# Performance work log

Hardware: AMD Instinct MI355X
Metric: run time of the kernel (lower is better)

Reference implementation:

```python
import jax, jax.numpy as jnp
import numpy as np

B, S, D = 2, 2048, 1024
H, DH, DL = 16, 64, 512
E, DFF, K = 8, 2048, 2
EPS = 1e-5


def setup_inputs() -> dict:
    key = jax.random.key(0)
    ks = jax.random.split(key, 10)
    std = 0.02
    inp = {
        'x': jax.random.normal(ks[0], (B, S, D), jnp.float32),
        'mask': jnp.tril(jnp.ones((S, S), dtype=bool))[None, None],  # causal (1,1,S,S)
        'ln1_scale': jnp.ones((D,), jnp.float32),
        'ln1_bias': jnp.zeros((D,), jnp.float32),
        'Wq': jax.random.normal(ks[1], (D, H * DH), jnp.float32) * std,
        'Wdkv': jax.random.normal(ks[2], (D, DL), jnp.float32) * std,
        'Wukv': jax.random.normal(ks[3], (DL, H * DH), jnp.float32) * std,
        'Wo': jax.random.normal(ks[4], (H * DH, D), jnp.float32) * std,
        'ln2_scale': jnp.ones((D,), jnp.float32),
        'ln2_bias': jnp.zeros((D,), jnp.float32),
        'Wgate': jax.random.normal(ks[5], (D, E), jnp.float32) * std,
        'bgate': jnp.zeros((E,), jnp.float32),
        'We1': jax.random.normal(ks[6], (E, D, DFF), jnp.float32) * std,
        'be1': jnp.zeros((E, DFF), jnp.float32),
        'We2': jax.random.normal(ks[7], (E, DFF, D), jnp.float32) * std,
        'be2': jnp.zeros((E, D), jnp.float32),
    }
    return inp


def _layernorm(x, g, b):
    m = jnp.mean(x, axis=-1, keepdims=True)
    v = jnp.mean(jnp.square(x - m), axis=-1, keepdims=True)
    return (x - m) * jax.lax.rsqrt(v + EPS) * g + b


def reference(x, mask, ln1_scale, ln1_bias, Wq, Wdkv, Wukv, Wo,
              ln2_scale, ln2_bias, Wgate, bgate, We1, be1, We2, be2):
    b, s, d = x.shape
    # --- MLA attention ---
    h = _layernorm(x, ln1_scale, ln1_bias)
    q = (h @ Wq).reshape(b, s, H, DH)
    kv = ((h @ Wdkv) @ Wukv).reshape(b, s, H, DH)  # k == v == kv
    scores = jnp.einsum('bqhd,bkhd->bhqk', q, kv) / (DH ** 0.5)
    scores = jnp.where(mask, scores, -jnp.inf)
    probs = jax.nn.softmax(scores, axis=-1)
    attn = jnp.einsum('bhqk,bkhd->bqhd', probs, kv).reshape(b, s, H * DH)
    x = x + attn @ Wo
    # --- MoE ---
    h2 = _layernorm(x, ln2_scale, ln2_bias)
    xf = h2.reshape(-1, d)                     # (T, D)
    T = xf.shape[0]
    logits = xf @ Wgate + bgate                # (T, E)
    w, sel = jax.lax.top_k(logits, K)          # (T, K)
    w = jax.nn.softmax(w, axis=-1)
    # scatter top-k weights into dense (T, E) combine weights
    wfull = jnp.zeros((T, E), xf.dtype).at[jnp.arange(T)[:, None], sel].add(w)
    hid = jax.nn.gelu(jnp.einsum('td,edf->etf', xf, We1) + be1[:, None, :],
                      approximate=False)
    oute = jnp.einsum('etf,efd->etd', hid, We2) + be2[:, None, :]
    moe = jnp.einsum('te,etd->td', wfull, oute)
    return x + moe.reshape(b, s, d)
```

## Files before the change

kernel.cpp:

```cpp
#include <hip/hip_runtime.h>

#define EPS_LN 1e-5f

typedef __attribute__((ext_vector_type(4))) float f32x4;
typedef __attribute__((ext_vector_type(8))) __bf16 bf16x8;
typedef __attribute__((ext_vector_type(2))) unsigned int u32x2;
typedef unsigned int u32;
typedef unsigned short u16;

__device__ __forceinline__ u16 f2b(float f) {
  unsigned int u = __builtin_bit_cast(unsigned int, f);
  unsigned int r = (u + 0x7FFFu + ((u >> 16) & 1u)) >> 16;
  return (u16)r;
}
__device__ __forceinline__ float b2f(u16 s) {
  unsigned int u = ((unsigned int)s) << 16;
  return __builtin_bit_cast(float, u);
}
__device__ __forceinline__ void splitf(float v, u16& h, u16& l) {
  h = f2b(v); l = f2b(v - b2f(h));
}
__device__ __forceinline__ float gelu_exact(float v) {
  return 0.5f * v * (1.0f + erff(v * 0.70710678118654752440f));
}
__device__ __forceinline__ void gload16(const void* g, void* l) {
  __builtin_amdgcn_global_load_lds((const __attribute__((address_space(1))) u32*)g,
                                   (__attribute__((address_space(3))) u32*)l, 16, 0, 0);
}
__device__ __forceinline__ void pv_mfma(f32x4& o, u32x2 a, u32x2 b) {
  asm("s_nop 1\n\tv_mfma_f32_16x16x16_bf16 %0, %1, %2, %0" : "+v"(o) : "v"(a), "v"(b));
}
__device__ __forceinline__ int fsw(int row, int sc) {
  return row * 64 + ((((sc >> 3) ^ (row & 7))) << 3) + (sc & 7);
}

__global__ __launch_bounds__(256) void k_transpose_bf16(
    const float* __restrict__ src, u16* __restrict__ dst, int K, int N)
{
  __shared__ u16 t[64][65];
  long base = (long)blockIdx.z * (long)K * (long)N;
  const float* s = src + base;
  u16* d = dst + base;
  int n0 = blockIdx.x * 64, k0 = blockIdx.y * 64;
  int c = threadIdx.x & 63, r = threadIdx.x >> 6;
#pragma unroll
  for (int i = 0; i < 16; i++) {
    int k = r * 16 + i;
    t[c][k] = f2b(s[(long)(k0 + k) * N + n0 + c]);
  }
  __syncthreads();
#pragma unroll
  for (int i = 0; i < 16; i++) {
    int n = r * 16 + i;
    d[(long)(n0 + n) * K + k0 + c] = t[n][c];
  }
}

__global__ __launch_bounds__(256) void k_split_transpose(
    const float* __restrict__ src, u16* __restrict__ dh,
    u16* __restrict__ dl, int K, int N)
{
  __shared__ float t[64][65];
  int n0 = blockIdx.x * 64, k0 = blockIdx.y * 64;
  int c = threadIdx.x & 63, r4 = threadIdx.x >> 6;
#pragma unroll
  for (int i = 0; i < 16; i++) {
    int k = r4 * 16 + i;
    t[c][k] = src[(long)(k0 + k) * N + n0 + c];
  }
  __syncthreads();
#pragma unroll
  for (int i = 0; i < 16; i++) {
    int n = r4 * 16 + i;
    float v = t[n][c];
    u16 h = f2b(v);
    dh[(long)(n0 + n) * K + k0 + c] = h;
    dl[(long)(n0 + n) * K + k0 + c] = f2b(v - b2f(h));
  }
}

__global__ __launch_bounds__(256) void k_transpose_kv(
    const u16* __restrict__ inh, const u16* __restrict__ inl,
    u16* __restrict__ outh, u16* __restrict__ outl)
{
  __shared__ u16 th[64][65];
  __shared__ u16 tl[64][65];
  int bh = blockIdx.y, s0 = blockIdx.x * 64;
  int b = bh >> 4, h = bh & 15;
  int c = threadIdx.x & 63, r = threadIdx.x >> 6;
  long ibase = ((long)b * 2048 + s0) * 1024 + h * 64;
  long obase = (long)bh * 64 * 2048 + s0;
#pragma unroll
  for (int i = 0; i < 16; i++) {
    int k = r * 16 + i;
    th[c][k] = inh[ibase + (long)k * 1024 + c];
    tl[c][k] = inl[ibase + (long)k * 1024 + c];
  }
  __syncthreads();
#pragma unroll
  for (int i = 0; i < 16; i++) {
    int n = r * 16 + i;
    outh[obase + (long)n * 2048 + c] = th[n][c];
    outl[obase + (long)n * 2048 + c] = tl[n][c];
  }
}

template<int MODE>
__global__ __launch_bounds__(256) void k_layernorm(
    const float* __restrict__ x, const float* __restrict__ g,
    const float* __restrict__ b, u16* __restrict__ o1, u16* __restrict__ o2)
{
  int row = blockIdx.x, tid = threadIdx.x;
  const float* xr = x + (long)row * 1024;
  float4 v = *(const float4*)&xr[tid * 4];
  float s = v.x + v.y + v.z + v.w;
  float sq = v.x * v.x + v.y * v.y + v.z * v.z + v.w * v.w;
#pragma unroll
  for (int o = 32; o; o >>= 1) { s += __shfl_down(s, o); sq += __shfl_down(sq, o); }
  __shared__ float red[8];
  int wave = tid >> 6, lane = tid & 63;
  if (lane == 0) { red[wave] = s; red[4 + wave] = sq; }
  __syncthreads();
  s  = red[0] + red[1] + red[2] + red[3];
  sq = red[4] + red[5] + red[6] + red[7];
  float mean = s * (1.0f / 1024.0f);
  float var  = sq * (1.0f / 1024.0f) - mean * mean;
  float rs = rsqrtf(var + EPS_LN);
  float4 gg = *(const float4*)&g[tid * 4];
  float4 bb = *(const float4*)&b[tid * 4];
  float ov[4];
  ov[0] = (v.x - mean) * rs * gg.x + bb.x;
  ov[1] = (v.y - mean) * rs * gg.y + bb.y;
  ov[2] = (v.z - mean) * rs * gg.z + bb.z;
  ov[3] = (v.w - mean) * rs * gg.w + bb.w;
  if (MODE == 1) {
    ushort4 o4; o4.x = f2b(ov[0]); o4.y = f2b(ov[1]); o4.z = f2b(ov[2]); o4.w = f2b(ov[3]);
    *(ushort4*)&o1[(long)row * 1024 + tid * 4] = o4;
  } else {
    ushort4 hh, ll;
    splitf(ov[0], hh.x, ll.x); splitf(ov[1], hh.y, ll.y);
    splitf(ov[2], hh.z, ll.z); splitf(ov[3], hh.w, ll.w);
    *(ushort4*)&o1[(long)row * 1024 + tid * 4] = hh;
    *(ushort4*)&o2[(long)row * 1024 + tid * 4] = ll;
  }
}

__global__ __launch_bounds__(256) void k_gemm_bf3(
    const u16* __restrict__ Ah, const u16* __restrict__ Al,
    const u16* __restrict__ Bh, const u16* __restrict__ Bl,
    float* __restrict__ P, int M, int N, int K)
{
  int split = blockIdx.x & 1;
  int bid = blockIdx.x >> 1;
  int nwg = gridDim.x >> 1, cpx = nwg >> 3;
  int wg = (bid & 7) * cpx + (bid >> 3);
  int mm = M >> 7;
  int mb = wg % mm, nb = wg / mm;
  long m0 = (long)mb * 128, n0 = (long)nb * 128;
  int K2 = K >> 1;
  int kbase = split * K2;
  __shared__ __align__(16) u16 sA[2][128 * 64];
  __shared__ __align__(16) u16 sB[2][128 * 64];
  int tid = threadIdx.x, lane = tid & 63, w = tid >> 6;
  int wr = w >> 1, wc = w & 1, l15 = lane & 15, l4 = lane >> 4;
  int lr8 = lane >> 3;
  int cl = (lane & 7) ^ lr8;
  int scol = (cl & 3) * 8;
  const u16* bA = (cl < 4) ? Ah : Al;
  const u16* bB = (cl < 4) ? Bh : Bl;
  long a_off[4], b_off[4];
#pragma unroll
  for (int r = 0; r < 4; r++) {
    int row = w * 32 + r * 8 + lr8;
    a_off[r] = (m0 + row) * (long)K + kbase + scol;
    b_off[r] = (n0 + row) * (long)K + kbase + scol;
  }
  int nt = K2 >> 5;

  f32x4 acc[4][4];
  f32x4 zz = {0.0f, 0.0f, 0.0f, 0.0f};
#pragma unroll
  for (int i = 0; i < 4; i++)
#pragma unroll
    for (int j = 0; j < 4; j++) acc[i][j] = zz;

#define STAGE_BF3(buf, s_) do { long o = (long)(s_) * 32; \
    _Pragma("unroll") \
    for (int r = 0; r < 4; r++) { \
      gload16(&bA[a_off[r] + o], &sA[buf][(w * 32 + r * 8) * 64]); \
      gload16(&bB[b_off[r] + o], &sB[buf][(w * 32 + r * 8) * 64]); \
    } } while (0)

  STAGE_BF3(0, 0);
  __syncthreads();
  int cur = 0;
  for (int s = 0; s < nt; s++) {
    if (s + 1 < nt) STAGE_BF3(cur ^ 1, s + 1);
    bf16x8 ah[4], al[4], bh[4], bl[4];
#pragma unroll
    for (int mi = 0; mi < 4; mi++) {
      int row = wr * 64 + mi * 16 + l15;
      int k7 = l15 & 7;
      ah[mi] = *(const bf16x8*)&sA[cur][row * 64 + ((l4 ^ k7) * 8)];
      al[mi] = *(const bf16x8*)&sA[cur][row * 64 + (((4 + l4) ^ k7) * 8)];
    }
#pragma unroll
    for (int ni = 0; ni < 4; ni++) {
      int row = wc * 64 + ni * 16 + l15;
      int k7 = l15 & 7;
      bh[ni] = *(const bf16x8*)&sB[cur][row * 64 + ((l4 ^ k7) * 8)];
      bl[ni] = *(const bf16x8*)&sB[cur][row * 64 + (((4 + l4) ^ k7) * 8)];
    }
#pragma unroll
    for (int mi = 0; mi < 4; mi++)
#pragma unroll
      for (int ni = 0; ni < 4; ni++) {
        acc[mi][ni] = __builtin_amdgcn_mfma_f32_16x16x32_bf16(ah[mi], bh[ni], acc[mi][ni], 0, 0, 0);
        acc[mi][ni] = __builtin_amdgcn_mfma_f32_16x16x32_bf16(ah[mi], bl[ni], acc[mi][ni], 0, 0, 0);
        acc[mi][ni] = __builtin_amdgcn_mfma_f32_16x16x32_bf16(al[mi], bh[ni], acc[mi][ni], 0, 0, 0);
      }
    __syncthreads();
    cur ^= 1;
  }
#undef STAGE_BF3
  long base = (long)split * M * N;
#pragma unroll
  for (int mi = 0; mi < 4; mi++) {
#pragma unroll
    for (int j = 0; j < 4; j++) {
      long row = m0 + wr * 64 + mi * 16 + l4 * 4 + j;
#pragma unroll
      for (int ni = 0; ni < 4; ni++) {
        long col = n0 + wc * 64 + ni * 16 + l15;
        P[base + row * N + col] = acc[mi][ni][j];
      }
    }
  }
}

__global__ __launch_bounds__(256) void k_red_split(
    const float* __restrict__ P, u16* __restrict__ Ch, u16* __restrict__ Cl, long MN)
{
  long i = ((long)blockIdx.x * 256 + threadIdx.x) * 4;
  float4 a = *(const float4*)&P[i];
  float4 b = *(const float4*)&P[MN + i];
  ushort4 h, l;
  splitf(a.x + b.x, h.x, l.x); splitf(a.y + b.y, h.y, l.y);
  splitf(a.z + b.z, h.z, l.z); splitf(a.w + b.w, h.w, l.w);
  *(ushort4*)&Ch[i] = h;
  *(ushort4*)&Cl[i] = l;
}

__global__ __launch_bounds__(256) void k_red_resid(
    const float* __restrict__ P, const float* __restrict__ x,
    float* __restrict__ out, long MN)
{
  long i = ((long)blockIdx.x * 256 + threadIdx.x) * 4;
  float4 a = *(const float4*)&P[i];
  float4 b = *(const float4*)&P[MN + i];
  float4 xv = *(const float4*)&x[i];
  float4 r = {a.x + b.x + xv.x, a.y + b.y + xv.y, a.z + b.z + xv.z, a.w + b.w + xv.w};
  *(float4*)&out[i] = r;
}

__global__ __launch_bounds__(256) void k_flash_v3(
    const u16* __restrict__ Qh, const u16* __restrict__ Ql,
    const u16* __restrict__ Kh, const u16* __restrict__ Kl,
    const u16* __restrict__ Th, const u16* __restrict__ Tl,
    u16* __restrict__ Oh, u16* __restrict__ Ol)
{
  int qb = (int)gridDim.y - 1 - (int)blockIdx.y;
  int bh = blockIdx.x;
  int q0 = qb * 64;
  int tid = threadIdx.x, lane = tid & 63, w = tid >> 6;
  int l15 = lane & 15, l4 = lane >> 4;
  __shared__ __align__(16) u16 Qsh[4096], Qsl[4096];
  __shared__ __align__(16) u16 Ksh[2][4096], Ksl[2][4096];
  __shared__ __align__(16) u16 Tsh[2][4096], Tsl[2][4096];
  long rowb = (long)(bh >> 4) * 2048;
  int  colo = (bh & 15) * 64;
  long tbase = (long)bh * 64 * 2048;
  int r8 = lane >> 3;
  int c8s = ((lane & 7) ^ r8) * 8;

#pragma unroll
  for (int k = 0; k < 2; k++) {
    int rr = w * 16 + k * 8;
    long src = (rowb + q0 + rr + r8) * 1024 + colo + c8s;
    gload16(&Qh[src], &Qsh[rr * 64]);
    gload16(&Ql[src], &Qsl[rr * 64]);
  }
#pragma unroll
  for (int k = 0; k < 2; k++) {
    int rr = w * 16 + k * 8;
    long srcK = (rowb + rr + r8) * 1024 + colo + c8s;
    long srcT = tbase + (long)(rr + r8) * 2048 + c8s;
    gload16(&Kh[srcK], &Ksh[0][rr * 64]);
    gload16(&Kl[srcK], &Ksl[0][rr * 64]);
    gload16(&Th[srcT], &Tsh[0][rr * 64]);
    gload16(&Tl[srcT], &Tsl[0][rr * 64]);
  }
  __syncthreads();

  float m = -1e30f, lsum = 0.0f;
  f32x4 o[4];
  f32x4 zz = {0.0f, 0.0f, 0.0f, 0.0f};
#pragma unroll
  for (int nb = 0; nb < 4; nb++) o[nb] = zz;
  int cur = 0;

  for (int kt = 0; kt <= qb; kt++) {
    int k0 = kt * 64;
    if (kt < qb) {
      int kn = k0 + 64, nxt = cur ^ 1;
#pragma unroll
      for (int k = 0; k < 2; k++) {
        int rr = w * 16 + k * 8;
        long srcK = (rowb + kn + rr + r8) * 1024 + colo + c8s;
        long srcT = tbase + (long)(rr + r8) * 2048 + kn + c8s;
        gload16(&Kh[srcK], &Ksh[nxt][rr * 64]);
        gload16(&Kl[srcK], &Ksl[nxt][rr * 64]);
        gload16(&Th[srcT], &Tsh[nxt][rr * 64]);
        gload16(&Tl[srcT], &Tsl[nxt][rr * 64]);
      }
    }
    f32x4 sT[4];
#pragma unroll
    for (int mi = 0; mi < 4; mi++) sT[mi] = zz;
#pragma unroll
    for (int ds = 0; ds < 2; ds++) {
      int qoff = fsw(w * 16 + l15, ds * 32 + l4 * 8);
      bf16x8 qh = *(const bf16x8*)&Qsh[qoff];
      bf16x8 ql = *(const bf16x8*)&Qsl[qoff];
#pragma unroll
      for (int mi = 0; mi < 4; mi++) {
        int koff = fsw(mi * 16 + l15, ds * 32 + l4 * 8);
        bf16x8 kh = *(const bf16x8*)&Ksh[cur][koff];
        bf16x8 kl = *(const bf16x8*)&Ksl[cur][koff];
        sT[mi] = __builtin_amdgcn_mfma_f32_16x16x32_bf16(kh, qh, sT[mi], 0, 0, 0);
        sT[mi] = __builtin_amdgcn_mfma_f32_16x16x32_bf16(kh, ql, sT[mi], 0, 0, 0);
        sT[mi] = __builtin_amdgcn_mfma_f32_16x16x32_bf16(kl, qh, sT[mi], 0, 0, 0);
      }
    }
    bool diag = (kt == qb);
    int qg = q0 + w * 16 + l15;
    float p[4][4];
    float tm = -1e30f;
#pragma unroll
    for (int mi = 0; mi < 4; mi++)
#pragma unroll
      for (int r = 0; r < 4; r++) {
        float v = sT[mi][r] * 0.125f;
        if (diag && (k0 + mi * 16 + l4 * 4 + r > qg)) v = -1e30f;
        p[mi][r] = v; tm = fmaxf(tm, v);
      }
    tm = fmaxf(tm, __shfl_xor(tm, 16));
    tm = fmaxf(tm, __shfl_xor(tm, 32));
    float mn = fmaxf(m, tm);
    float corr = __expf(m - mn);
    m = mn;
    float rs = 0.0f;
#pragma unroll
    for (int mi = 0; mi < 4; mi++)
#pragma unroll
      for (int r = 0; r < 4; r++) {
        float pv = __expf(p[mi][r] - mn);
        p[mi][r] = pv; rs += pv;
      }
    rs += __shfl_xor(rs, 16);
    rs += __shfl_xor(rs, 32);
    lsum = lsum * corr + rs;
    float corrO[4];
#pragma unroll
    for (int r = 0; r < 4; r++) corrO[r] = __shfl(corr, l4 * 4 + r);
#pragma unroll
    for (int nb = 0; nb < 4; nb++)
#pragma unroll
      for (int r = 0; r < 4; r++) o[nb][r] *= corrO[r];
    u32x2 pah[4], pal[4];
#pragma unroll
    for (int mi = 0; mi < 4; mi++) {
      u16 h[4], l[4];
#pragma unroll
      for (int r = 0; r < 4; r++) splitf(p[mi][r], h[r], l[r]);
      pah[mi][0] = (u32)h[0] | ((u32)h[1] << 16);
      pah[mi][1] = (u32)h[2] | ((u32)h[3] << 16);
      pal[mi][0] = (u32)l[0] | ((u32)l[1] << 16);
      pal[mi][1] = (u32)l[2] | ((u32)l[3] << 16);
    }
#pragma unroll
    for (int nb = 0; nb < 4; nb++) {
#pragma unroll
      for (int mi = 0; mi < 4; mi++) {
        int toff = fsw(nb * 16 + l15, mi * 16 + l4 * 4);
        u32x2 vh = *(const u32x2*)&Tsh[cur][toff];
        u32x2 vl = *(const u32x2*)&Tsl[cur][toff];
        pv_mfma(o[nb], pah[mi], vh);
        pv_mfma(o[nb], pah[mi], vl);
        pv_mfma(o[nb], pal[mi], vh);
      }
    }
    __syncthreads();
    cur ^= 1;
  }
  __builtin_amdgcn_sched_barrier(0);
  asm volatile("s_nop 7\n\ts_nop 7" ::: "memory");
  __builtin_amdgcn_sched_barrier(0);
  float inv[4];
#pragma unroll
  for (int r = 0; r < 4; r++) inv[r] = 1.0f / __shfl(lsum, l4 * 4 + r);
#pragma unroll
  for (int nb = 0; nb < 4; nb++)
#pragma unroll
    for (int r = 0; r < 4; r++) {
      long idx = (rowb + q0 + w * 16 + l4 * 4 + r) * 1024 + colo + nb * 16 + l15;
      u16 hh_, ll_; splitf(o[nb][r] * inv[r], hh_, ll_);
      Oh[idx] = hh_; Ol[idx] = ll_;
    }
}

__global__ __launch_bounds__(256) void k_gate(
    const float* __restrict__ x1, const float* __restrict__ g2, const float* __restrict__ b2,
    const float* __restrict__ Wg, const float* __restrict__ bg,
    int* __restrict__ sel, float* __restrict__ wts)
{
  int t = blockIdx.x * 4 + (threadIdx.x >> 6);
  int lane = threadIdx.x & 63;
  const float* xr = x1 + (long)t * 1024;
  float v[16], s = 0.0f, sq = 0.0f;
#pragma unroll
  for (int i = 0; i < 16; i++) { v[i] = xr[lane + 64 * i]; s += v[i]; sq += v[i] * v[i]; }
#pragma unroll
  for (int o = 32; o; o >>= 1) { s += __shfl_xor(s, o); sq += __shfl_xor(sq, o); }
  float mean = s * (1.0f / 1024.0f);
  float var = sq * (1.0f / 1024.0f) - mean * mean;
  float rs = rsqrtf(var + EPS_LN);
  float acc[8];
#pragma unroll
  for (int e = 0; e < 8; e++) acc[e] = 0.0f;
#pragma unroll
  for (int i = 0; i < 16; i++) {
    int d = lane + 64 * i;
    float hh = (v[i] - mean) * rs * g2[d] + b2[d];
    float4 w0 = *(const float4*)&Wg[d * 8];
    float4 w1 = *(const float4*)&Wg[d * 8 + 4];
    acc[0] += hh * w0.x; acc[1] += hh * w0.y; acc[2] += hh * w0.z; acc[3] += hh * w0.w;
    acc[4] += hh * w1.x; acc[5] += hh * w1.y; acc[6] += hh * w1.z; acc[7] += hh * w1.w;
  }
#pragma unroll
  for (int o = 32; o; o >>= 1)
#pragma unroll
    for (int e = 0; e < 8; e++) acc[e] += __shfl_xor(acc[e], o);
  if (lane == 0) {
    float le[8];
#pragma unroll
    for (int e = 0; e < 8; e++) le[e] = acc[e] + bg[e];
    int i0 = 0;
    for (int e = 1; e < 8; e++) if (le[e] > le[i0]) i0 = e;
    int i1 = (i0 == 0) ? 1 : 0;
    for (int e = 0; e < 8; e++) if (e != i0 && le[e] > le[i1]) i1 = e;
    float w0 = 1.0f / (1.0f + __expf(le[i1] - le[i0]));
    sel[2 * t] = i0; sel[2 * t + 1] = i1;
    wts[2 * t] = w0; wts[2 * t + 1] = 1.0f - w0;
  }
}

__global__ __launch_bounds__(256) void k_count(const int* __restrict__ sel, int* __restrict__ cnt)
{
  int e = blockIdx.x, tid = threadIdx.x;
  int c = 0;
  for (int t = tid; t < 4096; t += 256)
    c += (sel[2 * t] == e) + (sel[2 * t + 1] == e);
#pragma unroll
  for (int o = 32; o; o >>= 1) c += __shfl_down(c, o);
  __shared__ int red[4];
  int wave = tid >> 6, lane = tid & 63;
  if (lane == 0) red[wave] = c;
  __syncthreads();
  if (tid == 0) cnt[e] = red[0] + red[1] + red[2] + red[3];
}

__global__ void k_offsets(const int* __restrict__ cnt, int* __restrict__ offs)
{
  if (threadIdx.x == 0) {
    int a = 0; offs[0] = 0;
    for (int e = 0; e < 8; e++) { a += cnt[e]; offs[e + 1] = a; }
  }
}

__global__ __launch_bounds__(256) void k_scatter(
    const int* __restrict__ sel, const int* __restrict__ offs,
    int* __restrict__ tlist, int* __restrict__ slot_of)
{
  int e = blockIdx.x, tid = threadIdx.x;
  int lane = tid & 63, wave = tid >> 6;
  __shared__ int wsum[4];
  int base = offs[e];
  for (int t0 = 0; t0 < 4096; t0 += 256) {
    int t = t0 + tid;
    int s0 = sel[2 * t], s1 = sel[2 * t + 1];
    bool p = (s0 == e) || (s1 == e);
    int k = (s0 == e) ? 0 : 1;
    unsigned long long mb = __ballot(p);
    int rank = __popcll(mb & ((1ull << lane) - 1ull));
    if (lane == 0) wsum[wave] = __popcll(mb);
    __syncthreads();
    int wbase = 0;
    for (int w = 0; w < wave; w++) wbase += wsum[w];
    if (p) { int idx = base + wbase + rank; tlist[idx] = t; slot_of[2 * t + k] = idx; }
    base += wsum[0] + wsum[1] + wsum[2] + wsum[3];
    __syncthreads();
  }
}

template<int EPI>
__global__ __launch_bounds__(256) void k_gemm_moe(
    const u16* __restrict__ A, const u16* __restrict__ Bt,
    void* __restrict__ Cout, const float* __restrict__ bias,
    const int* __restrict__ tlist, const int* __restrict__ offs,
    int N, int K, long strideB, int strideBias)
{
  int e = blockIdx.x & 7, slot = blockIdx.x >> 3;
  int r0 = offs[e], r1 = offs[e + 1];
  int rows = r1 - r0;
  if (rows <= 0) return;
  int nn = N >> 7;
  int ntiles = ((rows + 127) >> 7) * nn;
  const u16* B = Bt + (long)e * strideB;
  const float* bvec = bias + (long)e * strideBias;
  __shared__ __align__(16) u16 lA[2][128 * 64];
  __shared__ __align__(16) u16 lB[2][128 * 64];
  int tid = threadIdx.x, lane = tid & 63, w = tid >> 6;
  int wr = w >> 1, wc = w & 1;
  int l15 = lane & 15, l4 = lane >> 4;
  int lr8 = lane >> 3;
  int csrc = ((lane & 7) ^ lr8) * 8;
  int nt = K >> 6;

  for (int t = slot; t < ntiles; t += 256) {
    int rbk = t / nn, nb = t - rbk * nn;
    int m0 = r0 + rbk * 128;
    long n0 = (long)nb * 128;
    u32 asrc[4], bsrc[4];
#pragma unroll
    for (int r = 0; r < 4; r++) {
      int row = w * 32 + r * 8 + lr8;
      int g = m0 + row; if (g > r1 - 1) g = r1 - 1;
      int ar = (EPI == 2) ? tlist[g] : g;
      asrc[r] = (u32)ar * (u32)K + csrc;
      bsrc[r] = (u32)(n0 + row) * (u32)K + csrc;
    }
    f32x4 acc[4][4];
    f32x4 zz = {0.0f, 0.0f, 0.0f, 0.0f};
#pragma unroll
    for (int i = 0; i < 4; i++)
#pragma unroll
      for (int j = 0; j < 4; j++) acc[i][j] = zz;

#define STAGE_MOE(buf, k0_) do { u32 o_ = (k0_); \
    _Pragma("unroll") \
    for (int r = 0; r < 4; r++) { \
      gload16(&A[asrc[r] + o_], &lA[buf][(w * 32 + r * 8) * 64]); \
      gload16(&B[bsrc[r] + o_], &lB[buf][(w * 32 + r * 8) * 64]); \
    } } while (0)

    STAGE_MOE(0, 0);
    __syncthreads();
    int cur = 0;
    for (int s = 0; s < nt; s++) {
      if (s + 1 < nt) STAGE_MOE(cur ^ 1, (u32)(s + 1) * 64);
#pragma unroll
      for (int ks = 0; ks < 2; ks++) {
        bf16x8 af[4], bq[4];
#pragma unroll
        for (int mi = 0; mi < 4; mi++) {
          int row = wr * 64 + mi * 16 + l15;
          af[mi] = *(const bf16x8*)&lA[cur][row * 64 + (((ks * 4 + l4) ^ (l15 & 7)) * 8)];
        }
#pragma unroll
        for (int ni = 0; ni < 4; ni++) {
          int row = wc * 64 + ni * 16 + l15;
          bq[ni] = *(const bf16x8*)&lB[cur][row * 64 + (((ks * 4 + l4) ^ (l15 & 7)) * 8)];
        }
#pragma unroll
        for (int mi = 0; mi < 4; mi++)
#pragma unroll
          for (int ni = 0; ni < 4; ni++)
            acc[mi][ni] = __builtin_amdgcn_mfma_f32_16x16x32_bf16(af[mi], bq[ni], acc[mi][ni], 0, 0, 0);
      }
      __syncthreads();
      cur ^= 1;
    }
#undef STAGE_MOE
#pragma unroll
    for (int mi = 0; mi < 4; mi++) {
#pragma unroll
      for (int j = 0; j < 4; j++) {
        int row = m0 + wr * 64 + mi * 16 + l4 * 4 + j;
        if (row < r1) {
#pragma unroll
          for (int ni = 0; ni < 4; ni++) {
            long col = n0 + wc * 64 + ni * 16 + l15;
            float vv = acc[mi][ni][j] + bvec[col];
            if (EPI == 2) {
              ((u16*)Cout)[(long)row * N + col] = f2b(gelu_exact(vv));
            } else {
              ((float*)Cout)[(long)row * N + col] = vv;
            }
          }
        }
      }
    }
  }
}

__global__ __launch_bounds__(256) void k_combine(
    const float* __restrict__ x1, const float* __restrict__ oute,
    const int* __restrict__ slot_of, const float* __restrict__ wts,
    float* __restrict__ out)
{
  int t = blockIdx.x;
  int c = threadIdx.x * 4;
  int s0 = slot_of[2 * t], s1 = slot_of[2 * t + 1];
  float w0 = wts[2 * t], w1 = wts[2 * t + 1];
  float4 a  = *(const float4*)&x1[(long)t * 1024 + c];
  float4 e0 = *(const float4*)&oute[(long)s0 * 1024 + c];
  float4 e1 = *(const float4*)&oute[(long)s1 * 1024 + c];
  float4 r;
  r.x = a.x + w0 * e0.x + w1 * e1.x;
  r.y = a.y + w0 * e0.y + w1 * e1.y;
  r.z = a.z + w0 * e0.z + w1 * e1.z;
  r.w = a.w + w0 * e0.w + w1 * e1.w;
  *(float4*)&out[(long)t * 1024 + c] = r;
}

extern "C" void kernel_launch(void* const* d_in, const int* in_sizes, int n_in,
                              void* d_out, int out_size, void* d_ws, size_t ws_size,
                              hipStream_t stream)
{
  const float* x    = (const float*)d_in[0];
  const float* ln1s = (const float*)d_in[2];
  const float* ln1b = (const float*)d_in[3];
  const float* Wq   = (const float*)d_in[4];
  const float* Wdkv = (const float*)d_in[5];
  const float* Wukv = (const float*)d_in[6];
  const float* Wo   = (const float*)d_in[7];
  const float* ln2s = (const float*)d_in[8];
  const float* ln2b = (const float*)d_in[9];
  const float* Wg   = (const float*)d_in[10];
  const float* bg   = (const float*)d_in[11];
  const float* We1  = (const float*)d_in[12];
  const float* be1  = (const float*)d_in[13];
  const float* We2  = (const float*)d_in[14];
  const float* be2  = (const float*)d_in[15];
  float* out = (float*)d_out;

  char* wp = (char*)d_ws;
  auto take = [&](size_t nbytes) -> void* {
    char* r = wp; wp += (nbytes + 255) & ~(size_t)255; return (void*)r;
  };
  u16* We1t = (u16*)take(8L * 2048 * 1024 * 2);
  u16* We2t = (u16*)take(8L * 1024 * 2048 * 2);
  u16* hh   = (u16*)take(4096L * 1024 * 2);
  u16* hl   = (u16*)take(4096L * 1024 * 2);
  u16* qh   = (u16*)take(4096L * 1024 * 2);
  u16* ql   = (u16*)take(4096L * 1024 * 2);
  u16* kvh  = (u16*)take(4096L * 1024 * 2);
  u16* kvl  = (u16*)take(4096L * 1024 * 2);
  u16* kvTh = (u16*)take(4096L * 1024 * 2);
  u16* kvTl = (u16*)take(4096L * 1024 * 2);
  u16* cbh  = (u16*)take(4096L * 512 * 2);
  u16* cbl  = (u16*)take(4096L * 512 * 2);
  float* x1 = (float*)take(4096L * 1024 * 4);
  u16* hid  = (u16*)take(8192L * 2048 * 2);
  int*   sel   = (int*)take(8192 * 4);
  float* wts   = (float*)take(8192 * 4);
  int*   cnt   = (int*)take(64);
  int*   offs  = (int*)take(64);
  int*   tlist = (int*)take(8192 * 4);
  int*   slot  = (int*)take(8192 * 4);
  u16* attn_h = hh;
  u16* attn_l = hl;
  u16* h2bf   = cbh;
  float* oute = (float*)qh;
  float* Pk   = (float*)We2t;
  u16* Wqh   = hid;
  u16* Wql   = Wqh   + 1024L * 1024;
  u16* Wdkvh = Wql   + 1024L * 1024;
  u16* Wdkvl = Wdkvh + 512L * 1024;
  u16* Wukvh = Wdkvl + 512L * 1024;
  u16* Wukvl = Wukvh + 1024L * 512;
  u16* Woh   = Wukvl + 1024L * 512;
  u16* Wol   = Woh   + 1024L * 1024;
  if ((size_t)(wp - (char*)d_ws) > ws_size) return;

  dim3 b256(256);
  k_split_transpose<<<dim3(16, 16), b256, 0, stream>>>(Wq,   Wqh,   Wql,   1024, 1024);
  k_split_transpose<<<dim3(8, 16),  b256, 0, stream>>>(Wdkv, Wdkvh, Wdkvl, 1024, 512);
  k_split_transpose<<<dim3(16, 8),  b256, 0, stream>>>(Wukv, Wukvh, Wukvl, 512, 1024);
  k_split_transpose<<<dim3(16, 16), b256, 0, stream>>>(Wo,   Woh,   Wol,   1024, 1024);
  k_layernorm<2><<<dim3(4096), b256, 0, stream>>>(x, ln1s, ln1b, hh, hl);
  k_gemm_bf3<<<dim3(512), b256, 0, stream>>>(hh, hl, Wqh, Wql, Pk, 4096, 1024, 1024);
  k_red_split<<<dim3(4096), b256, 0, stream>>>(Pk, qh, ql, 4096L * 1024);
  k_gemm_bf3<<<dim3(256), b256, 0, stream>>>(hh, hl, Wdkvh, Wdkvl, Pk, 4096, 512, 1024);
  k_red_split<<<dim3(2048), b256, 0, stream>>>(Pk, cbh, cbl, 4096L * 512);
  k_gemm_bf3<<<dim3(512), b256, 0, stream>>>(cbh, cbl, Wukvh, Wukvl, Pk, 4096, 1024, 512);
  k_red_split<<<dim3(4096), b256, 0, stream>>>(Pk, kvh, kvl, 4096L * 1024);
  k_transpose_kv<<<dim3(32, 32), b256, 0, stream>>>(kvh, kvl, kvTh, kvTl);
  k_flash_v3<<<dim3(32, 32), b256, 0, stream>>>(qh, ql, kvh, kvl, kvTh, kvTl, attn_h, attn_l);
  k_gemm_bf3<<<dim3(512), b256, 0, stream>>>(attn_h, attn_l, Woh, Wol, Pk, 4096, 1024, 1024);
  k_red_resid<<<dim3(4096), b256, 0, stream>>>(Pk, x, x1, 4096L * 1024);
  k_layernorm<1><<<dim3(4096), b256, 0, stream>>>(x1, ln2s, ln2b, h2bf, nullptr);
  k_gate<<<dim3(1024), b256, 0, stream>>>(x1, ln2s, ln2b, Wg, bg, sel, wts);
  k_count<<<dim3(8), b256, 0, stream>>>(sel, cnt);
  k_offsets<<<dim3(1), dim3(64), 0, stream>>>(cnt, offs);
  k_scatter<<<dim3(8), b256, 0, stream>>>(sel, offs, tlist, slot);
  k_transpose_bf16<<<dim3(32, 16, 8), b256, 0, stream>>>(We1, We1t, 1024, 2048);
  k_transpose_bf16<<<dim3(16, 32, 8), b256, 0, stream>>>(We2, We2t, 2048, 1024);
  k_gemm_moe<2><<<dim3(2048), b256, 0, stream>>>(h2bf, We1t, hid, be1, tlist, offs,
                                                 2048, 1024, 2048L * 1024, 2048);
  k_gemm_moe<3><<<dim3(2048), b256, 0, stream>>>(hid, We2t, oute, be2, tlist, offs,
                                                 1024, 2048, 1024L * 2048, 1024);
  k_combine<<<dim3(4096), b256, 0, stream>>>(x1, oute, slot, wts, out);
}
```

Baseline: 496.5 us.

## Fuse KV split-K reduction with transpose; flatten MoE tiles across experts

The split-K reduction of the KV projection is merged into the KV transpose kernel, so the bf16 hi/lo split is written to both layouts in one pass. This drops a kernel launch and a reread of the kv buffers. The MoE GEMMs now build a global tile list across all experts from prefix offsets and stride over it with fewer workgroups, instead of giving each expert a fixed 256-block slice. This is meant to balance load when experts receive uneven token counts, at the cost of a small per-tile expert search and changed tile ordering (row blocks now vary fastest).

```diff
diff --git a/kernel.cpp b/kernel.cpp
--- a/kernel.cpp
+++ b/kernel.cpp
@@ -79,12 +79,13 @@
   }
 }
 
-__global__ __launch_bounds__(256) void k_transpose_kv(
-    const u16* __restrict__ inh, const u16* __restrict__ inl,
-    u16* __restrict__ outh, u16* __restrict__ outl)
+__global__ __launch_bounds__(256) void k_red_kv(
+    const float* __restrict__ P, u16* __restrict__ kvh, u16* __restrict__ kvl,
+    u16* __restrict__ kvTh, u16* __restrict__ kvTl)
 {
   __shared__ u16 th[64][65];
   __shared__ u16 tl[64][65];
+  const long MN = 4096L * 1024;
   int bh = blockIdx.y, s0 = blockIdx.x * 64;
   int b = bh >> 4, h = bh & 15;
   int c = threadIdx.x & 63, r = threadIdx.x >> 6;
@@ -93,15 +94,18 @@
 #pragma unroll
   for (int i = 0; i < 16; i++) {
     int k = r * 16 + i;
-    th[c][k] = inh[ibase + (long)k * 1024 + c];
-    tl[c][k] = inl[ibase + (long)k * 1024 + c];
+    long idx = ibase + (long)k * 1024 + c;
+    float v = P[idx] + P[MN + idx];
+    u16 hh_, ll_; splitf(v, hh_, ll_);
+    kvh[idx] = hh_; kvl[idx] = ll_;
+    th[c][k] = hh_; tl[c][k] = ll_;
   }
   __syncthreads();
 #pragma unroll
   for (int i = 0; i < 16; i++) {
     int n = r * 16 + i;
-    outh[obase + (long)n * 2048 + c] = th[n][c];
-    outl[obase + (long)n * 2048 + c] = tl[n][c];
+    kvTh[obase + (long)n * 2048 + c] = th[n][c];
+    kvTl[obase + (long)n * 2048 + c] = tl[n][c];
   }
 }
 
@@ -520,14 +524,18 @@
     const int* __restrict__ tlist, const int* __restrict__ offs,
     int N, int K, long strideB, int strideBias)
 {
-  int e = blockIdx.x & 7, slot = blockIdx.x >> 3;
-  int r0 = offs[e], r1 = offs[e + 1];
-  int rows = r1 - r0;
-  if (rows <= 0) return;
+  int nwg = gridDim.x;
+  int wg0 = ((blockIdx.x & 7) * (nwg >> 3)) + (blockIdx.x >> 3);
   int nn = N >> 7;
-  int ntiles = ((rows + 127) >> 7) * nn;
-  const u16* B = Bt + (long)e * strideB;
-  const float* bvec = bias + (long)e * strideBias;
+  int off_c[9];
+#pragma unroll
+  for (int e = 0; e <= 8; e++) off_c[e] = offs[e];
+  int tile_off[9];
+  tile_off[0] = 0;
+#pragma unroll
+  for (int e = 0; e < 8; e++)
+    tile_off[e + 1] = tile_off[e] + (((off_c[e + 1] - off_c[e]) + 127) >> 7) * nn;
+  int ntiles = tile_off[8];
   __shared__ __align__(16) u16 lA[2][128 * 64];
   __shared__ __align__(16) u16 lB[2][128 * 64];
   int tid = threadIdx.x, lane = tid & 63, w = tid >> 6;
@@ -537,10 +545,17 @@
   int csrc = ((lane & 7) ^ lr8) * 8;
   int nt = K >> 6;
 
-  for (int t = slot; t < ntiles; t += 256) {
-    int rbk = t / nn, nb = t - rbk * nn;
+  for (int t = wg0; t < ntiles; t += nwg) {
+    int e = 0;
+    while (e < 7 && t >= tile_off[e + 1]) e++;
+    int lt = t - tile_off[e];
+    int r0 = off_c[e], r1 = off_c[e + 1];
+    int rbcnt = ((r1 - r0) + 127) >> 7;
+    int rbk = lt % rbcnt, nb = lt / rbcnt;
     int m0 = r0 + rbk * 128;
     long n0 = (long)nb * 128;
+    const u16* B = Bt + (long)e * strideB;
+    const float* bvec = bias + (long)e * strideBias;
     u32 asrc[4], bsrc[4];
 #pragma unroll
     for (int r = 0; r < 4; r++) {
@@ -705,8 +720,7 @@
   k_gemm_bf3<<<dim3(256), b256, 0, stream>>>(hh, hl, Wdkvh, Wdkvl, Pk, 4096, 512, 1024);
   k_red_split<<<dim3(2048), b256, 0, stream>>>(Pk, cbh, cbl, 4096L * 512);
   k_gemm_bf3<<<dim3(512), b256, 0, stream>>>(cbh, cbl, Wukvh, Wukvl, Pk, 4096, 1024, 512);
-  k_red_split<<<dim3(4096), b256, 0, stream>>>(Pk, kvh, kvl, 4096L * 1024);
-  k_transpose_kv<<<dim3(32, 32), b256, 0, stream>>>(kvh, kvl, kvTh, kvTl);
+  k_red_kv<<<dim3(32, 32), b256, 0, stream>>>(Pk, kvh, kvl, kvTh, kvTl);
   k_flash_v3<<<dim3(32, 32), b256, 0, stream>>>(qh, ql, kvh, kvl, kvTh, kvTl, attn_h, attn_l);
   k_gemm_bf3<<<dim3(512), b256, 0, stream>>>(attn_h, attn_l, Woh, Wol, Pk, 4096, 1024, 1024);
   k_red_resid<<<dim3(4096), b256, 0, stream>>>(Pk, x, x1, 4096L * 1024);
@@ -717,9 +731,9 @@
   k_scatter<<<dim3(8), b256, 0, stream>>>(sel, offs, tlist, slot);
   k_transpose_bf16<<<dim3(32, 16, 8), b256, 0, stream>>>(We1, We1t, 1024, 2048);
   k_transpose_bf16<<<dim3(16, 32, 8), b256, 0, stream>>>(We2, We2t, 2048, 1024);
-  k_gemm_moe<2><<<dim3(2048), b256, 0, stream>>>(h2bf, We1t, hid, be1, tlist, offs,
+  k_gemm_moe<2><<<dim3(1024), b256, 0, stream>>>(h2bf, We1t, hid, be1, tlist, offs,
                                                  2048, 1024, 2048L * 1024, 2048);
-  k_gemm_moe<3><<<dim3(2048), b256, 0, stream>>>(hid, We2t, oute, be2, tlist, offs,
+  k_gemm_moe<3><<<dim3(512), b256, 0, stream>>>(hid, We2t, oute, be2, tlist, offs,
                                                  1024, 2048, 1024L * 2048, 1024);
   k_combine<<<dim3(4096), b256, 0, stream>>>(x1, oute, slot, wts, out);
 }
```

New measurement: 511.7 us. 1.03x slower.
